# Kernel optimization log

Measured on AMD Instinct MI355X. Metric: run time of the kernel, lower is better.

Reference implementation:

```python
import jax, jax.numpy as jnp
import numpy as np
import math

D_MODEL = 1024
N_HEADS = 16
N_QUBITS = 8
HEAD_DIM = D_MODEL // N_HEADS
B, L = 2, 2048


def setup_inputs() -> dict:
    key = jax.random.key(0)
    ks = jax.random.split(key, 16)
    s = 0.02
    return {
        "query": jax.random.normal(ks[0], (B, L, D_MODEL), jnp.float32),
        "key_": jax.random.normal(ks[1], (B, L, D_MODEL), jnp.float32),
        "value": jax.random.normal(ks[2], (B, L, D_MODEL), jnp.float32),
        "Wq": jax.random.normal(ks[3], (D_MODEL, D_MODEL), jnp.float32) * s,
        "bq": jnp.zeros((D_MODEL,), jnp.float32),
        "Wk": jax.random.normal(ks[4], (D_MODEL, D_MODEL), jnp.float32) * s,
        "bk": jnp.zeros((D_MODEL,), jnp.float32),
        "Wv": jax.random.normal(ks[5], (D_MODEL, D_MODEL), jnp.float32) * s,
        "bv": jnp.zeros((D_MODEL,), jnp.float32),
        "Wo": jax.random.normal(ks[6], (D_MODEL, D_MODEL), jnp.float32) * s,
        "bo": jnp.zeros((D_MODEL,), jnp.float32),
        "Wf": jax.random.normal(ks[7], (HEAD_DIM, N_QUBITS), jnp.float32) * s,  # feature map weight (input->qubits)
        "bf": jnp.zeros((N_QUBITS,), jnp.float32),
        "quantum_weights": jax.random.normal(ks[8], (N_HEADS, N_QUBITS), jnp.float32) * 0.1,
        "entanglement_strength": jnp.asarray(0.5, jnp.float32),
    }


def _heads(x):
    # [B, L, D] -> [B, H, L, head_dim]
    b, l, _ = x.shape
    return x.reshape(b, l, N_HEADS, HEAD_DIM).transpose(0, 2, 1, 3)


def reference(query, key_, value, Wq, bq, Wk, bk, Wv, bv, Wo, bo, Wf, bf, quantum_weights, entanglement_strength):
    Qh = _heads(query @ Wq.T + bq)   # [B,H,L,d]
    Kh = _heads(key_ @ Wk.T + bk)
    Vh = _heads(value @ Wv.T + bv)

    classical = jnp.einsum("bhid,bhjd->bhij", Qh, Kh) / math.sqrt(HEAD_DIM)

    # quantum feature map: tanh(linear) -> [B,H,L,Q]
    qq = jnp.tanh(jnp.einsum("bhld,dq->bhlq", Qh, Wf) + bf)
    kq = jnp.tanh(jnp.einsum("bhld,dq->bhlq", Kh, Wf) + bf)

    # mean_q w_q*cos(qq_i - kq_j) == (1/Q)[(w*cos qq)@cos(kq)^T + (w*sin qq)@sin(kq)^T]
    w = jax.nn.sigmoid(quantum_weights)[None, :, None, :]  # [1,H,1,Q]
    quantum = (
        jnp.einsum("bhiq,bhjq->bhij", jnp.cos(qq) * w, jnp.cos(kq))
        + jnp.einsum("bhiq,bhjq->bhij", jnp.sin(qq) * w, jnp.sin(kq))
    ) / N_QUBITS
    ent = jax.nn.sigmoid(entanglement_strength)
    quantum = quantum * ent

    mix = ent  # same sigmoid(entanglement_strength) used as mixing weight
    combined = (1.0 - mix) * classical + mix * quantum

    attn = jax.nn.softmax(combined, axis=-1)  # [B,H,L,L]
    attended = jnp.einsum("bhij,bhjd->bhid", attn, Vh)
    attended = attended.transpose(0, 2, 1, 3).reshape(query.shape[0], query.shape[1], D_MODEL)
    output = attended @ Wo.T + bo
    return output, attn.mean(axis=1)
```

## Files before the change

kernel.cpp:

```cpp
#include <hip/hip_runtime.h>


typedef unsigned short u16;
typedef unsigned int u32;
typedef short v8s __attribute__((ext_vector_type(8)));
typedef float v4f __attribute__((ext_vector_type(4)));

static __device__ __forceinline__ float b2f(u16 h) {
  union { u32 u; float f; } a; a.u = ((u32)h) << 16; return a.f;
}
static __device__ __forceinline__ u16 f2b(float f) {
  union { float f; u32 u; } a; a.f = f;
  u32 u = a.u;
  u32 r = u + 0x7FFFu + ((u >> 16) & 1u);
  return (u16)(r >> 16);
}
static __device__ __forceinline__ u32 fbits(float f) {
  union { float f; u32 u; } a; a.f = f; return a.u;
}
static __device__ __forceinline__ v4f mfma16(v8s a, v8s b, v4f c) {
  return __builtin_amdgcn_mfma_f32_16x16x32_bf16(a, b, c, 0, 0, 0);
}

__global__ __launch_bounds__(256) void k_f2b(const float* __restrict__ x, u16* __restrict__ y, int n4) {
  int i = blockIdx.x * 256 + threadIdx.x;
  if (i >= n4) return;
  float4 v = ((const float4*)x)[i];
  union { u16 s[4]; uint2 u; } o;
  o.s[0] = f2b(v.x); o.s[1] = f2b(v.y); o.s[2] = f2b(v.z); o.s[3] = f2b(v.w);
  ((uint2*)y)[i] = o.u;
}

__global__ __launch_bounds__(256) void k_gemm_bt(const u16* __restrict__ A, const u16* __restrict__ Bm,
                                                 const float* __restrict__ bias,
                                                 float* __restrict__ Cf, u16* __restrict__ Cb,
                                                 u16* __restrict__ Ct,
                                                 int M, int N, int K) {
  __shared__ __align__(16) u16 As[64][48];
  __shared__ __align__(16) u16 Bs[64][48];
  __shared__ __align__(16) u16 Ts[64][70];
  int t = threadIdx.x, w = t >> 6, lane = t & 63, quad = lane >> 4, l16 = lane & 15;
  int m0 = blockIdx.y * 64, n0 = blockIdx.x * 64;
  int srow = t >> 2, scol = (t & 3) * 8;
  v4f zf = {0.f, 0.f, 0.f, 0.f};
  v4f acc[4]; acc[0] = zf; acc[1] = zf; acc[2] = zf; acc[3] = zf;

  for (int k0 = 0; k0 < K; k0 += 32) {
    __syncthreads();
    *(uint4*)&As[srow][scol] = *(const uint4*)&A[(size_t)(m0 + srow) * K + k0 + scol];
    *(uint4*)&Bs[srow][scol] = *(const uint4*)&Bm[(size_t)(n0 + srow) * K + k0 + scol];
    __syncthreads();
    v8s af = *(const v8s*)&As[w * 16 + l16][quad * 8];
#pragma unroll
    for (int n16 = 0; n16 < 4; ++n16) {
      v8s bfr = *(const v8s*)&Bs[n16 * 16 + l16][quad * 8];
      acc[n16] = mfma16(af, bfr, acc[n16]);
    }
  }
  if (Ct) {
    __syncthreads();
#pragma unroll
    for (int n16 = 0; n16 < 4; ++n16)
#pragma unroll
      for (int r = 0; r < 4; ++r)
        Ts[w * 16 + quad * 4 + r][n16 * 16 + l16] = f2b(acc[n16][r] + bias[n0 + n16 * 16 + l16]);
    __syncthreads();
    int cc = t >> 2, seg = t & 3;
    union { uint4 u[2]; u16 s[16]; } ob;
#pragma unroll
    for (int e = 0; e < 16; ++e) ob.s[e] = Ts[seg * 16 + e][cc];
    int bb = m0 >> 11, ml = m0 & 2047;
    u16* dst = Ct + ((size_t)(bb * 1024 + n0 + cc)) * 2048 + ml + seg * 16;
    *(uint4*)dst = ob.u[0];
    *(uint4*)(dst + 8) = ob.u[1];
  } else {
#pragma unroll
    for (int n16 = 0; n16 < 4; ++n16) {
#pragma unroll
      for (int r = 0; r < 4; ++r) {
        int rr = m0 + w * 16 + quad * 4 + r;
        int cc = n0 + n16 * 16 + l16;
        float v = acc[n16][r] + bias[cc];
        if (Cf) Cf[(size_t)rr * N + cc] = v;
        else    Cb[(size_t)rr * N + cc] = f2b(v);
      }
    }
  }
}

__global__ __launch_bounds__(256) void k_features(const u16* __restrict__ P, const float* __restrict__ Wf,
                                                  const float* __restrict__ bff, const float* __restrict__ qw,
                                                  const float* __restrict__ entp, u16* __restrict__ Out, int isK) {
  int idx = blockIdx.x * 256 + threadIdx.x;
  int b = idx >> 15, h = (idx >> 11) & 15, l = idx & 2047;
  const u16* src = P + ((size_t)(b * 2048 + l)) * 1024 + h * 64;
  u16* dst = Out + (size_t)idx * 96;
  float x[64];
#pragma unroll
  for (int g = 0; g < 8; ++g) {
    union { uint4 u; u16 s[8]; } uu;
    uu.u = *(const uint4*)(src + g * 8);
#pragma unroll
    for (int e = 0; e < 8; ++e) x[g * 8 + e] = b2f(uu.s[e]);
  }
  float qv[8];
#pragma unroll
  for (int q = 0; q < 8; ++q) {
    float a = bff[q];
    for (int d = 0; d < 64; ++d) a += x[d] * Wf[d * 8 + q];
    qv[q] = tanhf(a);
  }
  float ent = 1.f / (1.f + __expf(-entp[0]));
  if (!isK) {
#pragma unroll
    for (int g = 0; g < 8; ++g) *(uint4*)(dst + g * 8) = *(const uint4*)(src + g * 8);
#pragma unroll
    for (int q = 0; q < 8; ++q) {
      float sw = 1.f / (1.f + __expf(-qw[h * 8 + q]));
      dst[64 + q] = f2b(cosf(qv[q]) * sw);
      dst[72 + q] = f2b(sinf(qv[q]) * sw);
    }
  } else {
    float c1 = (1.f - ent) * 0.125f, c2 = ent * ent * 0.125f;
#pragma unroll
    for (int d = 0; d < 64; ++d) dst[d] = f2b(x[d] * c1);
#pragma unroll
    for (int q = 0; q < 8; ++q) {
      dst[64 + q] = f2b(cosf(qv[q]) * c2);
      dst[72 + q] = f2b(sinf(qv[q]) * c2);
    }
  }
#pragma unroll
  for (int e = 80; e < 96; ++e) dst[e] = 0;
}

__global__ __launch_bounds__(512) void k_flash(const u16* __restrict__ Qa, const u16* __restrict__ Ka,
                                               const u16* __restrict__ VtG, u16* __restrict__ At,
                                               float* __restrict__ lb) {
  __shared__ __align__(16) u16 Ks[64][104];
  __shared__ __align__(16) u16 Vt[64][72];
  __shared__ __align__(16) u16 Ps[8][16][72];

  int t = threadIdx.x, w = t >> 6, lane = t & 63, quad = lane >> 4, l16 = lane & 15;
  int i0 = blockIdx.x * 128, h = blockIdx.y, b = blockIdx.z;
  size_t qbase = ((size_t)(b * 16 + h)) * 2048 * 96;
  const u16* Qrow = Qa + qbase + (size_t)(i0 + w * 16 + l16) * 96;
  v8s aq[3];
#pragma unroll
  for (int ks = 0; ks < 3; ++ks) aq[ks] = *(const v8s*)(Qrow + ks * 32 + quad * 8);

  const u16* Kbase = Ka + qbase;
  const u16* Vbase = VtG + ((size_t)(b * 1024 + h * 64)) * 2048;

  int r0 = t / 12, c0 = t % 12;
  const u16* g0 = Kbase + r0 * 96 + c0 * 8;
  u16* d0 = &Ks[r0][c0 * 8];
  int idx1 = t + 512;
  const u16* g1; u16* d1; int adv1;
  if (idx1 < 768) {
    int r1 = idx1 / 12, c1 = idx1 % 12;
    g1 = Kbase + r1 * 96 + c1 * 8; d1 = &Ks[r1][c1 * 8]; adv1 = 6144;
  } else {
    int vi = idx1 - 768;
    g1 = Vbase + (vi >> 3) * 2048 + (vi & 7) * 8; d1 = &Vt[vi >> 3][(vi & 7) * 8]; adv1 = 64;
  }
  int vi2 = t + 1024 - 768;
  const u16* g2 = Vbase + (vi2 >> 3) * 2048 + (vi2 & 7) * 8;
  u16* d2 = &Vt[vi2 >> 3][(vi2 & 7) * 8];

  v4f zf = {0.f, 0.f, 0.f, 0.f};
  v4f oacc[4]; oacc[0] = zf; oacc[1] = zf; oacc[2] = zf; oacc[3] = zf;
  float l_acc = 0.f;

  uint4 f0 = *(const uint4*)g0;
  uint4 f1 = *(const uint4*)g1;
  uint4 f2 = {0, 0, 0, 0};
  if (t < 256) f2 = *(const uint4*)g2;

  for (int j0 = 0; j0 < 2048; j0 += 64) {
    *(uint4*)d0 = f0;
    *(uint4*)d1 = f1;
    if (t < 256) *(uint4*)d2 = f2;
    __syncthreads();
    g0 += 6144; g1 += adv1; g2 += 64;
    if (j0 + 64 < 2048) {
      f0 = *(const uint4*)g0;
      f1 = *(const uint4*)g1;
      if (t < 256) f2 = *(const uint4*)g2;
    }

    v4f sacc[4]; sacc[0] = zf; sacc[1] = zf; sacc[2] = zf; sacc[3] = zf;
#pragma unroll
    for (int j16 = 0; j16 < 4; ++j16)
#pragma unroll
      for (int ks = 0; ks < 3; ++ks) {
        v8s kf = *(const v8s*)&Ks[j16 * 16 + l16][ks * 32 + quad * 8];
        sacc[j16] = mfma16(kf, aq[ks], sacc[j16]);
      }

#pragma unroll
    for (int j16 = 0; j16 < 4; ++j16) {
      float e0 = __expf(sacc[j16][0]);
      float e1 = __expf(sacc[j16][1]);
      float e2 = __expf(sacc[j16][2]);
      float e3 = __expf(sacc[j16][3]);
      l_acc += (e0 + e1) + (e2 + e3);
      u32 x0 = fbits(e0) + 0x8000u, x1 = fbits(e1) + 0x8000u;
      u32 x2 = fbits(e2) + 0x8000u, x3 = fbits(e3) + 0x8000u;
      uint2 pp;
      pp.x = __builtin_amdgcn_perm(x1, x0, 0x07060302u);
      pp.y = __builtin_amdgcn_perm(x3, x2, 0x07060302u);
      *(uint2*)&Ps[w][l16][j16 * 16 + quad * 4] = pp;
    }
#pragma unroll
    for (int jh = 0; jh < 2; ++jh) {
      v8s pf = *(const v8s*)&Ps[w][l16][jh * 32 + quad * 8];
#pragma unroll
      for (int d16 = 0; d16 < 4; ++d16) {
        v8s vf = *(const v8s*)&Vt[d16 * 16 + l16][jh * 32 + quad * 8];
        oacc[d16] = mfma16(pf, vf, oacc[d16]);
      }
    }
    __syncthreads();
  }

  l_acc += __shfl_xor(l_acc, 16, 64);
  l_acc += __shfl_xor(l_acc, 32, 64);
  float linv = 1.f / l_acc;
#pragma unroll
  for (int r = 0; r < 4; ++r) {
    float li = __shfl(linv, quad * 4 + r, 64);
    int ri = i0 + w * 16 + quad * 4 + r;
#pragma unroll
    for (int d16 = 0; d16 < 4; ++d16)
      At[((size_t)(b * 2048 + ri)) * 1024 + h * 64 + d16 * 16 + l16] = f2b(oacc[d16][r] * li);
  }
  if (lane < 16) {
    size_t mbase = ((size_t)(b * 16 + h)) * 2048;
    lb[mbase + i0 + w * 16 + lane] = l_acc;
  }
}

__global__ __launch_bounds__(256) void k_pass2(const u16* __restrict__ Qa, const u16* __restrict__ Ka,
                                               const float* __restrict__ lb,
                                               float* __restrict__ out1) {
  __shared__ __align__(16) u16 Ks[64][104];
  __shared__ float Ls[16][128];
  int t = threadIdx.x, w = t >> 6, lane = t & 63, quad = lane >> 4, l16 = lane & 15;
  int j0 = blockIdx.x * 64, i0 = blockIdx.y * 128, b = blockIdx.z;

#pragma unroll
  for (int rep = 0; rep < 8; ++rep) {
    int idx = t + rep * 256;
    int hh = idx >> 7, il = idx & 127;
    Ls[hh][il] = 0.0625f / lb[((size_t)(b * 16 + hh)) * 2048 + i0 + il];
  }

  size_t base0 = (size_t)b * 16 * 2048 * 96;
  const u16* kg[3]; u16* kd[3];
#pragma unroll
  for (int rep = 0; rep < 3; ++rep) {
    int idx = t + rep * 256;
    int r_ = idx / 12, c_ = idx % 12;
    kg[rep] = Ka + base0 + (size_t)(j0 + r_) * 96 + c_ * 8;
    kd[rep] = &Ks[r_][c_ * 8];
  }
  uint4 f0 = *(const uint4*)kg[0];
  uint4 f1 = *(const uint4*)kg[1];
  uint4 f2 = *(const uint4*)kg[2];

  const u16* q0 = Qa + base0 + (size_t)(i0 + w * 32 + l16) * 96 + quad * 8;
  const u16* q1 = q0 + 16 * 96;

  v4f zf = {0.f, 0.f, 0.f, 0.f};
  v4f macc[2][4];
#pragma unroll
  for (int i16 = 0; i16 < 2; ++i16)
#pragma unroll
    for (int j16 = 0; j16 < 4; ++j16) macc[i16][j16] = zf;

  v8s a[2][3];
#pragma unroll
  for (int ks = 0; ks < 3; ++ks) {
    a[0][ks] = *(const v8s*)(q0 + ks * 32);
    a[1][ks] = *(const v8s*)(q1 + ks * 32);
  }

  for (int h = 0; h < 16; ++h) {
    *(uint4*)kd[0] = f0;
    *(uint4*)kd[1] = f1;
    *(uint4*)kd[2] = f2;
    __syncthreads();
    if (h < 15) {
      kg[0] += 196608; kg[1] += 196608; kg[2] += 196608;
      f0 = *(const uint4*)kg[0];
      f1 = *(const uint4*)kg[1];
      f2 = *(const uint4*)kg[2];
    }

    v4f sacc[2][4];
#pragma unroll
    for (int i16 = 0; i16 < 2; ++i16)
#pragma unroll
      for (int j16 = 0; j16 < 4; ++j16) sacc[i16][j16] = zf;
#pragma unroll
    for (int ks = 0; ks < 3; ++ks)
#pragma unroll
      for (int j16 = 0; j16 < 4; ++j16) {
        v8s kf = *(const v8s*)&Ks[j16 * 16 + l16][ks * 32 + quad * 8];
        sacc[0][j16] = mfma16(a[0][ks], kf, sacc[0][j16]);
        sacc[1][j16] = mfma16(a[1][ks], kf, sacc[1][j16]);
      }

    if (h < 15) {
      q0 += 196608; q1 += 196608;
#pragma unroll
      for (int ks = 0; ks < 3; ++ks) {
        a[0][ks] = *(const v8s*)(q0 + ks * 32);
        a[1][ks] = *(const v8s*)(q1 + ks * 32);
      }
    }

    float li[2][4];
#pragma unroll
    for (int i16 = 0; i16 < 2; ++i16)
#pragma unroll
      for (int r = 0; r < 4; ++r)
        li[i16][r] = Ls[h][w * 32 + i16 * 16 + quad * 4 + r];
#pragma unroll
    for (int i16 = 0; i16 < 2; ++i16)
#pragma unroll
      for (int j16 = 0; j16 < 4; ++j16)
#pragma unroll
        for (int r = 0; r < 4; ++r)
          macc[i16][j16][r] += __expf(sacc[i16][j16][r]) * li[i16][r];
    __syncthreads();
  }

  float* o = out1 + (size_t)b * 2048 * 2048;
#pragma unroll
  for (int i16 = 0; i16 < 2; ++i16)
#pragma unroll
    for (int j16 = 0; j16 < 4; ++j16)
#pragma unroll
      for (int r = 0; r < 4; ++r)
        o[(size_t)(i0 + w * 32 + i16 * 16 + quad * 4 + r) * 2048 + j0 + j16 * 16 + l16] =
            macc[i16][j16][r];
}

extern "C" void kernel_launch(void* const* d_in, const int* in_sizes, int n_in,
                              void* d_out, int out_size, void* d_ws, size_t ws_size,
                              hipStream_t stream) {
  (void)in_sizes; (void)n_in; (void)out_size; (void)ws_size;
  const float* query = (const float*)d_in[0];
  const float* key_  = (const float*)d_in[1];
  const float* value = (const float*)d_in[2];
  const float* Wq = (const float*)d_in[3];
  const float* bq = (const float*)d_in[4];
  const float* Wk = (const float*)d_in[5];
  const float* bk = (const float*)d_in[6];
  const float* Wv = (const float*)d_in[7];
  const float* bv = (const float*)d_in[8];
  const float* Wo = (const float*)d_in[9];
  const float* bo = (const float*)d_in[10];
  const float* Wf = (const float*)d_in[11];
  const float* bff = (const float*)d_in[12];
  const float* qw = (const float*)d_in[13];
  const float* entp = (const float*)d_in[14];

  char* p = (char*)d_ws;
  u16* Xq  = (u16*)(p + 0);
  u16* Xk  = (u16*)(p + 8388608);
  u16* Xv  = (u16*)(p + 16777216);
  u16* Wqb = (u16*)(p + 25165824);
  u16* Wkb = (u16*)(p + 27262976);
  u16* Wvb = (u16*)(p + 29360128);
  u16* Wob = (u16*)(p + 31457280);
  u16* Qp  = (u16*)(p + 33554432);
  u16* Kp  = (u16*)(p + 41943040);
  u16* VtG = (u16*)(p + 50331648);
  u16* Qaa = (u16*)(p + 58720256);
  u16* Kaa = (u16*)(p + 71303168);
  float* lb = (float*)(p + 84148224);
  u16* At  = (u16*)(p + 84410368);

  k_f2b<<<4096, 256, 0, stream>>>(query, Xq, 1048576);
  k_f2b<<<4096, 256, 0, stream>>>(key_,  Xk, 1048576);
  k_f2b<<<4096, 256, 0, stream>>>(value, Xv, 1048576);
  k_f2b<<<1024, 256, 0, stream>>>(Wq, Wqb, 262144);
  k_f2b<<<1024, 256, 0, stream>>>(Wk, Wkb, 262144);
  k_f2b<<<1024, 256, 0, stream>>>(Wv, Wvb, 262144);
  k_f2b<<<1024, 256, 0, stream>>>(Wo, Wob, 262144);

  dim3 gg(16, 64);
  k_gemm_bt<<<gg, 256, 0, stream>>>(Xq, Wqb, bq, nullptr, Qp, nullptr, 4096, 1024, 1024);
  k_gemm_bt<<<gg, 256, 0, stream>>>(Xk, Wkb, bk, nullptr, Kp, nullptr, 4096, 1024, 1024);
  k_gemm_bt<<<gg, 256, 0, stream>>>(Xv, Wvb, bv, nullptr, nullptr, VtG, 4096, 1024, 1024);

  k_features<<<256, 256, 0, stream>>>(Qp, Wf, bff, qw, entp, Qaa, 0);
  k_features<<<256, 256, 0, stream>>>(Kp, Wf, bff, qw, entp, Kaa, 1);

  k_flash<<<dim3(16, 16, 2), 512, 0, stream>>>(Qaa, Kaa, VtG, At, lb);

  k_pass2<<<dim3(32, 16, 2), 256, 0, stream>>>(Qaa, Kaa, lb, (float*)d_out + 4194304);

  k_gemm_bt<<<gg, 256, 0, stream>>>(At, Wob, bo, (float*)d_out, nullptr, nullptr, 4096, 1024, 1024);
}
```

Measured before the change: 387.5 us.

## Use 128x128 GEMM tiles with direct-to-LDS loads, batch QKV projections, widen flash rows

Replaces the 64x64 GEMM with a 128x128 tiled kernel in which each wave computes a 64x64 sub-tile, and tiles are loaded through global_load_lds straight into shared memory. The three Q/K/V projections now run as one launch selected by blockIdx.z. The flash kernel now uses 256 threads, each wave handling 32 query rows, so every K/V fragment read from LDS is reused across two row blocks. The aim is more data reuse per LDS read and fewer launches, at the cost of higher register pressure and fewer blocks in flight.

```diff
diff --git a/kernel.cpp b/kernel.cpp
--- a/kernel.cpp
+++ b/kernel.cpp
@@ -20,6 +20,10 @@
 }
 static __device__ __forceinline__ v4f mfma16(v8s a, v8s b, v4f c) {
   return __builtin_amdgcn_mfma_f32_16x16x32_bf16(a, b, c, 0, 0, 0);
+}
+static __device__ __forceinline__ void gload16(const u16* g, u16* l) {
+  __builtin_amdgcn_global_load_lds((const __attribute__((address_space(1))) u32*)g,
+                                   (__attribute__((address_space(3))) u32*)l, 16, 0, 0);
 }
 
 __global__ __launch_bounds__(256) void k_f2b(const float* __restrict__ x, u16* __restrict__ y, int n4) {
@@ -31,60 +35,103 @@
   ((uint2*)y)[i] = o.u;
 }
 
-__global__ __launch_bounds__(256) void k_gemm_bt(const u16* __restrict__ A, const u16* __restrict__ Bm,
-                                                 const float* __restrict__ bias,
-                                                 float* __restrict__ Cf, u16* __restrict__ Cb,
-                                                 u16* __restrict__ Ct,
-                                                 int M, int N, int K) {
-  __shared__ __align__(16) u16 As[64][48];
-  __shared__ __align__(16) u16 Bs[64][48];
-  __shared__ __align__(16) u16 Ts[64][70];
+__global__ __launch_bounds__(256) void k_gemm128(
+    const u16* __restrict__ A0, const u16* __restrict__ A1, const u16* __restrict__ A2,
+    const u16* __restrict__ B0, const u16* __restrict__ B1, const u16* __restrict__ B2,
+    const float* __restrict__ bias0, const float* __restrict__ bias1, const float* __restrict__ bias2,
+    u16* __restrict__ O0, u16* __restrict__ O1, u16* __restrict__ O2t,
+    float* __restrict__ Cf) {
+  __shared__ __align__(16) u16 As[128 * 32];
+  __shared__ __align__(16) u16 Bs[128 * 32];
+  __shared__ __align__(16) u16 Ts[4][64][68];
+  const int K = 1024, N = 1024;
   int t = threadIdx.x, w = t >> 6, lane = t & 63, quad = lane >> 4, l16 = lane & 15;
-  int m0 = blockIdx.y * 64, n0 = blockIdx.x * 64;
-  int srow = t >> 2, scol = (t & 3) * 8;
+  int z = blockIdx.z;
+  const u16* A = (z == 0) ? A0 : (z == 1) ? A1 : A2;
+  const u16* Bm = (z == 0) ? B0 : (z == 1) ? B1 : B2;
+  const float* bias = (z == 0) ? bias0 : (z == 1) ? bias1 : bias2;
+  int n0 = blockIdx.x * 128, m0 = blockIdx.y * 128;
+
+  int srow = lane >> 2, scol = (lane & 3) * 8;
+  const u16 *ga[2], *gb[2];
+  u16 *la[2], *lbp[2];
+#pragma unroll
+  for (int p = 0; p < 2; ++p) {
+    int row = p * 64 + w * 16 + srow;
+    ga[p] = A + (size_t)(m0 + row) * K + scol;
+    gb[p] = Bm + (size_t)(n0 + row) * K + scol;
+    la[p] = As + (p * 256 + w * 64) * 8;
+    lbp[p] = Bs + (p * 256 + w * 64) * 8;
+  }
+
+  int mrow = (w >> 1) * 64, ncol = (w & 1) * 64;
   v4f zf = {0.f, 0.f, 0.f, 0.f};
-  v4f acc[4]; acc[0] = zf; acc[1] = zf; acc[2] = zf; acc[3] = zf;
+  v4f acc[4][4];
+#pragma unroll
+  for (int mi = 0; mi < 4; ++mi)
+#pragma unroll
+    for (int ni = 0; ni < 4; ++ni) acc[mi][ni] = zf;
 
   for (int k0 = 0; k0 < K; k0 += 32) {
     __syncthreads();
-    *(uint4*)&As[srow][scol] = *(const uint4*)&A[(size_t)(m0 + srow) * K + k0 + scol];
-    *(uint4*)&Bs[srow][scol] = *(const uint4*)&Bm[(size_t)(n0 + srow) * K + k0 + scol];
-    __syncthreads();
-    v8s af = *(const v8s*)&As[w * 16 + l16][quad * 8];
-#pragma unroll
-    for (int n16 = 0; n16 < 4; ++n16) {
-      v8s bfr = *(const v8s*)&Bs[n16 * 16 + l16][quad * 8];
-      acc[n16] = mfma16(af, bfr, acc[n16]);
-    }
-  }
-  if (Ct) {
-    __syncthreads();
-#pragma unroll
-    for (int n16 = 0; n16 < 4; ++n16)
-#pragma unroll
-      for (int r = 0; r < 4; ++r)
-        Ts[w * 16 + quad * 4 + r][n16 * 16 + l16] = f2b(acc[n16][r] + bias[n0 + n16 * 16 + l16]);
-    __syncthreads();
-    int cc = t >> 2, seg = t & 3;
-    union { uint4 u[2]; u16 s[16]; } ob;
-#pragma unroll
-    for (int e = 0; e < 16; ++e) ob.s[e] = Ts[seg * 16 + e][cc];
+#pragma unroll
+    for (int p = 0; p < 2; ++p) {
+      gload16(ga[p] + k0, la[p]);
+      gload16(gb[p] + k0, lbp[p]);
+    }
+    __syncthreads();
+    v8s af[4], bfr[4];
+#pragma unroll
+    for (int x = 0; x < 4; ++x) {
+      af[x] = *(const v8s*)&As[(mrow + x * 16 + l16) * 32 + quad * 8];
+      bfr[x] = *(const v8s*)&Bs[(ncol + x * 16 + l16) * 32 + quad * 8];
+    }
+#pragma unroll
+    for (int mi = 0; mi < 4; ++mi)
+#pragma unroll
+      for (int ni = 0; ni < 4; ++ni)
+        acc[mi][ni] = mfma16(af[mi], bfr[ni], acc[mi][ni]);
+  }
+
+  float bv[4];
+#pragma unroll
+  for (int ni = 0; ni < 4; ++ni) bv[ni] = bias[n0 + ncol + ni * 16 + l16];
+
+  if (Cf) {
+#pragma unroll
+    for (int mi = 0; mi < 4; ++mi)
+#pragma unroll
+      for (int ni = 0; ni < 4; ++ni)
+#pragma unroll
+        for (int r = 0; r < 4; ++r)
+          Cf[(size_t)(m0 + mrow + mi * 16 + quad * 4 + r) * N + n0 + ncol + ni * 16 + l16] =
+              acc[mi][ni][r] + bv[ni];
+  } else if (z != 2) {
+    u16* O = z ? O1 : O0;
+#pragma unroll
+    for (int mi = 0; mi < 4; ++mi)
+#pragma unroll
+      for (int ni = 0; ni < 4; ++ni)
+#pragma unroll
+        for (int r = 0; r < 4; ++r)
+          O[(size_t)(m0 + mrow + mi * 16 + quad * 4 + r) * N + n0 + ncol + ni * 16 + l16] =
+              f2b(acc[mi][ni][r] + bv[ni]);
+  } else {
+#pragma unroll
+    for (int mi = 0; mi < 4; ++mi)
+#pragma unroll
+      for (int ni = 0; ni < 4; ++ni)
+#pragma unroll
+        for (int r = 0; r < 4; ++r)
+          Ts[w][mi * 16 + quad * 4 + r][ni * 16 + l16] = f2b(acc[mi][ni][r] + bv[ni]);
+    int c = lane;
+    union { uint4 u[8]; u16 s[64]; } cb;
+#pragma unroll
+    for (int e = 0; e < 64; ++e) cb.s[e] = Ts[w][e][c];
     int bb = m0 >> 11, ml = m0 & 2047;
-    u16* dst = Ct + ((size_t)(bb * 1024 + n0 + cc)) * 2048 + ml + seg * 16;
-    *(uint4*)dst = ob.u[0];
-    *(uint4*)(dst + 8) = ob.u[1];
-  } else {
-#pragma unroll
-    for (int n16 = 0; n16 < 4; ++n16) {
-#pragma unroll
-      for (int r = 0; r < 4; ++r) {
-        int rr = m0 + w * 16 + quad * 4 + r;
-        int cc = n0 + n16 * 16 + l16;
-        float v = acc[n16][r] + bias[cc];
-        if (Cf) Cf[(size_t)rr * N + cc] = v;
-        else    Cb[(size_t)rr * N + cc] = f2b(v);
-      }
-    }
+    u16* dst = O2t + ((size_t)(bb * 1024 + n0 + ncol + c)) * 2048 + ml + mrow;
+#pragma unroll
+    for (int e = 0; e < 8; ++e) *(uint4*)(dst + e * 8) = cb.u[e];
   }
 }
 
@@ -134,110 +181,130 @@
   for (int e = 80; e < 96; ++e) dst[e] = 0;
 }
 
-__global__ __launch_bounds__(512) void k_flash(const u16* __restrict__ Qa, const u16* __restrict__ Ka,
+__global__ __launch_bounds__(256) void k_flash(const u16* __restrict__ Qa, const u16* __restrict__ Ka,
                                                const u16* __restrict__ VtG, u16* __restrict__ At,
                                                float* __restrict__ lb) {
   __shared__ __align__(16) u16 Ks[64][104];
   __shared__ __align__(16) u16 Vt[64][72];
-  __shared__ __align__(16) u16 Ps[8][16][72];
+  __shared__ __align__(16) u16 Ps[4][2][16][72];
 
   int t = threadIdx.x, w = t >> 6, lane = t & 63, quad = lane >> 4, l16 = lane & 15;
   int i0 = blockIdx.x * 128, h = blockIdx.y, b = blockIdx.z;
   size_t qbase = ((size_t)(b * 16 + h)) * 2048 * 96;
-  const u16* Qrow = Qa + qbase + (size_t)(i0 + w * 16 + l16) * 96;
-  v8s aq[3];
-#pragma unroll
-  for (int ks = 0; ks < 3; ++ks) aq[ks] = *(const v8s*)(Qrow + ks * 32 + quad * 8);
-
+  v8s aq[2][3];
+#pragma unroll
+  for (int i16 = 0; i16 < 2; ++i16) {
+    const u16* Qrow = Qa + qbase + (size_t)(i0 + w * 32 + i16 * 16 + l16) * 96;
+#pragma unroll
+    for (int ks = 0; ks < 3; ++ks) aq[i16][ks] = *(const v8s*)(Qrow + ks * 32 + quad * 8);
+  }
   const u16* Kbase = Ka + qbase;
   const u16* Vbase = VtG + ((size_t)(b * 1024 + h * 64)) * 2048;
 
-  int r0 = t / 12, c0 = t % 12;
-  const u16* g0 = Kbase + r0 * 96 + c0 * 8;
-  u16* d0 = &Ks[r0][c0 * 8];
-  int idx1 = t + 512;
-  const u16* g1; u16* d1; int adv1;
-  if (idx1 < 768) {
-    int r1 = idx1 / 12, c1 = idx1 % 12;
-    g1 = Kbase + r1 * 96 + c1 * 8; d1 = &Ks[r1][c1 * 8]; adv1 = 6144;
-  } else {
-    int vi = idx1 - 768;
-    g1 = Vbase + (vi >> 3) * 2048 + (vi & 7) * 8; d1 = &Vt[vi >> 3][(vi & 7) * 8]; adv1 = 64;
-  }
-  int vi2 = t + 1024 - 768;
-  const u16* g2 = Vbase + (vi2 >> 3) * 2048 + (vi2 & 7) * 8;
-  u16* d2 = &Vt[vi2 >> 3][(vi2 & 7) * 8];
+  const u16 *kg[3], *vg[2];
+  u16 *kd[3], *vd[2];
+#pragma unroll
+  for (int p = 0; p < 3; ++p) {
+    int idx = t + p * 256, r_ = idx / 12, c_ = idx % 12;
+    kg[p] = Kbase + (size_t)r_ * 96 + c_ * 8;
+    kd[p] = &Ks[r_][c_ * 8];
+  }
+#pragma unroll
+  for (int p = 0; p < 2; ++p) {
+    int idx = t + p * 256, d_ = idx >> 3, c_ = (idx & 7) * 8;
+    vg[p] = Vbase + (size_t)d_ * 2048 + c_;
+    vd[p] = &Vt[d_][c_];
+  }
 
   v4f zf = {0.f, 0.f, 0.f, 0.f};
-  v4f oacc[4]; oacc[0] = zf; oacc[1] = zf; oacc[2] = zf; oacc[3] = zf;
-  float l_acc = 0.f;
-
-  uint4 f0 = *(const uint4*)g0;
-  uint4 f1 = *(const uint4*)g1;
-  uint4 f2 = {0, 0, 0, 0};
-  if (t < 256) f2 = *(const uint4*)g2;
+  v4f oacc[2][4];
+#pragma unroll
+  for (int i16 = 0; i16 < 2; ++i16)
+#pragma unroll
+    for (int d16 = 0; d16 < 4; ++d16) oacc[i16][d16] = zf;
+  float l_acc[2] = {0.f, 0.f};
+
+  uint4 fk0 = *(const uint4*)kg[0];
+  uint4 fk1 = *(const uint4*)kg[1];
+  uint4 fk2 = *(const uint4*)kg[2];
+  uint4 fv0 = *(const uint4*)vg[0];
+  uint4 fv1 = *(const uint4*)vg[1];
 
   for (int j0 = 0; j0 < 2048; j0 += 64) {
-    *(uint4*)d0 = f0;
-    *(uint4*)d1 = f1;
-    if (t < 256) *(uint4*)d2 = f2;
-    __syncthreads();
-    g0 += 6144; g1 += adv1; g2 += 64;
+    *(uint4*)kd[0] = fk0;
+    *(uint4*)kd[1] = fk1;
+    *(uint4*)kd[2] = fk2;
+    *(uint4*)vd[0] = fv0;
+    *(uint4*)vd[1] = fv1;
+    __syncthreads();
+    kg[0] += 6144; kg[1] += 6144; kg[2] += 6144; vg[0] += 64; vg[1] += 64;
     if (j0 + 64 < 2048) {
-      f0 = *(const uint4*)g0;
-      f1 = *(const uint4*)g1;
-      if (t < 256) f2 = *(const uint4*)g2;
-    }
-
-    v4f sacc[4]; sacc[0] = zf; sacc[1] = zf; sacc[2] = zf; sacc[3] = zf;
+      fk0 = *(const uint4*)kg[0];
+      fk1 = *(const uint4*)kg[1];
+      fk2 = *(const uint4*)kg[2];
+      fv0 = *(const uint4*)vg[0];
+      fv1 = *(const uint4*)vg[1];
+    }
+
+    v4f sacc[2][4];
+#pragma unroll
+    for (int i16 = 0; i16 < 2; ++i16)
+#pragma unroll
+      for (int j16 = 0; j16 < 4; ++j16) sacc[i16][j16] = zf;
 #pragma unroll
     for (int j16 = 0; j16 < 4; ++j16)
 #pragma unroll
       for (int ks = 0; ks < 3; ++ks) {
         v8s kf = *(const v8s*)&Ks[j16 * 16 + l16][ks * 32 + quad * 8];
-        sacc[j16] = mfma16(kf, aq[ks], sacc[j16]);
+        sacc[0][j16] = mfma16(kf, aq[0][ks], sacc[0][j16]);
+        sacc[1][j16] = mfma16(kf, aq[1][ks], sacc[1][j16]);
       }
 
 #pragma unroll
-    for (int j16 = 0; j16 < 4; ++j16) {
-      float e0 = __expf(sacc[j16][0]);
-      float e1 = __expf(sacc[j16][1]);
-      float e2 = __expf(sacc[j16][2]);
-      float e3 = __expf(sacc[j16][3]);
-      l_acc += (e0 + e1) + (e2 + e3);
-      u32 x0 = fbits(e0) + 0x8000u, x1 = fbits(e1) + 0x8000u;
-      u32 x2 = fbits(e2) + 0x8000u, x3 = fbits(e3) + 0x8000u;
-      uint2 pp;
-      pp.x = __builtin_amdgcn_perm(x1, x0, 0x07060302u);
-      pp.y = __builtin_amdgcn_perm(x3, x2, 0x07060302u);
-      *(uint2*)&Ps[w][l16][j16 * 16 + quad * 4] = pp;
-    }
+    for (int i16 = 0; i16 < 2; ++i16)
+#pragma unroll
+      for (int j16 = 0; j16 < 4; ++j16) {
+        float e0 = __expf(sacc[i16][j16][0]);
+        float e1 = __expf(sacc[i16][j16][1]);
+        float e2 = __expf(sacc[i16][j16][2]);
+        float e3 = __expf(sacc[i16][j16][3]);
+        l_acc[i16] += (e0 + e1) + (e2 + e3);
+        uint2 pp;
+        pp.x = __builtin_amdgcn_perm(fbits(e1) + 0x8000u, fbits(e0) + 0x8000u, 0x07060302u);
+        pp.y = __builtin_amdgcn_perm(fbits(e3) + 0x8000u, fbits(e2) + 0x8000u, 0x07060302u);
+        *(uint2*)&Ps[w][i16][l16][j16 * 16 + quad * 4] = pp;
+      }
 #pragma unroll
     for (int jh = 0; jh < 2; ++jh) {
-      v8s pf = *(const v8s*)&Ps[w][l16][jh * 32 + quad * 8];
+      v8s pf0 = *(const v8s*)&Ps[w][0][l16][jh * 32 + quad * 8];
+      v8s pf1 = *(const v8s*)&Ps[w][1][l16][jh * 32 + quad * 8];
 #pragma unroll
       for (int d16 = 0; d16 < 4; ++d16) {
         v8s vf = *(const v8s*)&Vt[d16 * 16 + l16][jh * 32 + quad * 8];
-        oacc[d16] = mfma16(pf, vf, oacc[d16]);
+        oacc[0][d16] = mfma16(pf0, vf, oacc[0][d16]);
+        oacc[1][d16] = mfma16(pf1, vf, oacc[1][d16]);
       }
     }
     __syncthreads();
   }
 
-  l_acc += __shfl_xor(l_acc, 16, 64);
-  l_acc += __shfl_xor(l_acc, 32, 64);
-  float linv = 1.f / l_acc;
-#pragma unroll
-  for (int r = 0; r < 4; ++r) {
-    float li = __shfl(linv, quad * 4 + r, 64);
-    int ri = i0 + w * 16 + quad * 4 + r;
-#pragma unroll
-    for (int d16 = 0; d16 < 4; ++d16)
-      At[((size_t)(b * 2048 + ri)) * 1024 + h * 64 + d16 * 16 + l16] = f2b(oacc[d16][r] * li);
-  }
-  if (lane < 16) {
-    size_t mbase = ((size_t)(b * 16 + h)) * 2048;
-    lb[mbase + i0 + w * 16 + lane] = l_acc;
+#pragma unroll
+  for (int i16 = 0; i16 < 2; ++i16) {
+    l_acc[i16] += __shfl_xor(l_acc[i16], 16, 64);
+    l_acc[i16] += __shfl_xor(l_acc[i16], 32, 64);
+    float linv = 1.f / l_acc[i16];
+#pragma unroll
+    for (int r = 0; r < 4; ++r) {
+      float li = __shfl(linv, quad * 4 + r, 64);
+      int ri = i0 + w * 32 + i16 * 16 + quad * 4 + r;
+#pragma unroll
+      for (int d16 = 0; d16 < 4; ++d16)
+        At[((size_t)(b * 2048 + ri)) * 1024 + h * 64 + d16 * 16 + l16] = f2b(oacc[i16][d16][r] * li);
+    }
+    if (lane < 16) {
+      size_t mbase = ((size_t)(b * 16 + h)) * 2048;
+      lb[mbase + i0 + w * 32 + i16 * 16 + lane] = l_acc[i16];
+    }
   }
 }
 
@@ -392,17 +459,16 @@
   k_f2b<<<1024, 256, 0, stream>>>(Wv, Wvb, 262144);
   k_f2b<<<1024, 256, 0, stream>>>(Wo, Wob, 262144);
 
-  dim3 gg(16, 64);
-  k_gemm_bt<<<gg, 256, 0, stream>>>(Xq, Wqb, bq, nullptr, Qp, nullptr, 4096, 1024, 1024);
-  k_gemm_bt<<<gg, 256, 0, stream>>>(Xk, Wkb, bk, nullptr, Kp, nullptr, 4096, 1024, 1024);
-  k_gemm_bt<<<gg, 256, 0, stream>>>(Xv, Wvb, bv, nullptr, nullptr, VtG, 4096, 1024, 1024);
+  k_gemm128<<<dim3(8, 32, 3), 256, 0, stream>>>(Xq, Xk, Xv, Wqb, Wkb, Wvb, bq, bk, bv,
+                                                Qp, Kp, VtG, nullptr);
 
   k_features<<<256, 256, 0, stream>>>(Qp, Wf, bff, qw, entp, Qaa, 0);
   k_features<<<256, 256, 0, stream>>>(Kp, Wf, bff, qw, entp, Kaa, 1);
 
-  k_flash<<<dim3(16, 16, 2), 512, 0, stream>>>(Qaa, Kaa, VtG, At, lb);
+  k_flash<<<dim3(16, 16, 2), 256, 0, stream>>>(Qaa, Kaa, VtG, At, lb);
 
   k_pass2<<<dim3(32, 16, 2), 256, 0, stream>>>(Qaa, Kaa, lb, (float*)d_out + 4194304);
 
-  k_gemm_bt<<<gg, 256, 0, stream>>>(At, Wob, bo, (float*)d_out, nullptr, nullptr, 4096, 1024, 1024);
-}
+  k_gemm128<<<dim3(8, 32, 1), 256, 0, stream>>>(At, At, At, Wob, Wob, Wob, bo, bo, bo,
+                                                nullptr, nullptr, nullptr, (float*)d_out);
+}
```

New measurement: 359.9 us. 1.08x faster.
